# Performance work log

Measured on AMD Instinct MI355X. Metric: run time of the kernel, lower is better.

The kernel has to match this reference:

```python
import jax, jax.numpy as jnp
import numpy as np

N_NODES = 100000
N_EDGES = 3200000
NUM_TYPES = 8
TYPE_DIM = 16
IN_DIM = 5
HID = 64
HEADS = 2
OUT = 64
LN_EPS = 1e-5
NEG_SLOPE = 0.2


def segment_softmax(logits, seg, num_segments):
    # logits: [E, H], seg: [E] destination ids
    m = jax.ops.segment_max(logits, seg, num_segments=num_segments)
    m = jnp.where(jnp.isfinite(m), m, 0.0)
    e = jnp.exp(logits - m[seg])
    s = jax.ops.segment_sum(e, seg, num_segments=num_segments)
    return e / (s[seg] + 1e-16)


def gat_conv(x, W, a_src, a_dst, b, src, dst, n_nodes, heads, ch):
    # x: [N, F_in], W: [F_in, heads*ch], a_src/a_dst: [heads, ch], b: [heads*ch]
    h = (x @ W).reshape(n_nodes, heads, ch)            # [N, H, C]
    al_s = jnp.einsum('nhc,hc->nh', h, a_src)          # [N, H]
    al_d = jnp.einsum('nhc,hc->nh', h, a_dst)          # [N, H]
    e = jax.nn.leaky_relu(al_s[src] + al_d[dst], NEG_SLOPE)  # [E, H]
    alpha = segment_softmax(e, dst, n_nodes)           # [E, H]
    msg = alpha[:, :, None] * h[src]                   # [E, H, C]
    out = jax.ops.segment_sum(msg, dst, num_segments=n_nodes)  # [N, H, C]
    return out.reshape(n_nodes, heads * ch) + b


def setup_inputs() -> dict:
    key = jax.random.key(0)
    ks = jax.random.split(key, 16)
    in1 = IN_DIM + TYPE_DIM  # 21
    inp = {
        'x': jax.random.normal(ks[0], (N_NODES, IN_DIM), dtype=jnp.float32),
        'edge_index': jax.random.randint(ks[1], (2, N_EDGES), 0, N_NODES, dtype=jnp.int32),
        'type_ids': jax.random.randint(ks[2], (N_NODES,), 0, NUM_TYPES, dtype=jnp.int32),
        'type_emb': jax.random.normal(ks[3], (NUM_TYPES, TYPE_DIM), dtype=jnp.float32) * 0.3,
        'W1': jax.random.normal(ks[4], (in1, HID), dtype=jnp.float32) * (1.0 / np.sqrt(in1)),
        'a_src1': jax.random.normal(ks[5], (HEADS, HID // HEADS), dtype=jnp.float32) * 0.1,
        'a_dst1': jax.random.normal(ks[6], (HEADS, HID // HEADS), dtype=jnp.float32) * 0.1,
        'b1': jnp.zeros((HID,), dtype=jnp.float32),
        'W2': jax.random.normal(ks[7], (HID, OUT), dtype=jnp.float32) * (1.0 / np.sqrt(HID)),
        'a_src2': jax.random.normal(ks[8], (1, OUT), dtype=jnp.float32) * 0.1,
        'a_dst2': jax.random.normal(ks[9], (1, OUT), dtype=jnp.float32) * 0.1,
        'b2': jnp.zeros((OUT,), dtype=jnp.float32),
        'gamma': jnp.ones((OUT,), dtype=jnp.float32),
        'beta': jnp.zeros((OUT,), dtype=jnp.float32),
    }
    return inp


def reference(x, type_emb, W1, a_src1, a_dst1, b1, W2, a_src2, a_dst2, b2, gamma, beta, edge_index, type_ids):
    n = x.shape[0]
    # type embedding concat
    xin = jnp.concatenate([x, type_emb[type_ids]], axis=1)  # [N, 21]
    # add self loops (PyG GATConv default)
    loops = jnp.arange(n, dtype=edge_index.dtype)
    src = jnp.concatenate([edge_index[0], loops])
    dst = jnp.concatenate([edge_index[1], loops])
    h = gat_conv(xin, W1, a_src1, a_dst1, b1, src, dst, n, HEADS, HID // HEADS)
    h = jax.nn.relu(h)  # dropout = identity at inference
    h = gat_conv(h, W2, a_src2, a_dst2, b2, src, dst, n, 1, OUT)
    # LayerNorm
    mu = jnp.mean(h, axis=-1, keepdims=True)
    var = jnp.var(h, axis=-1, keepdims=True)
    return (h - mu) / jnp.sqrt(var + LN_EPS) * gamma + beta
```

## Files before the change

kernel.cpp:

```cpp
#include <hip/hip_runtime.h>
#include <hip/hip_fp16.h>

#define NEG_SLOPE 0.2f
#define BKT_SHIFT 8
#define BKT_NODES 256
#define BKT_CAP 10240
#define SRC_SHIFT 18
#define SRC_MASK 0x3FFFF
#define CHUNK 8192
#define NBMAX 512

typedef _Float16 half8 __attribute__((ext_vector_type(8)));
typedef float float4v __attribute__((ext_vector_type(4)));

__device__ __forceinline__ int wave_iscan(int v, int lane) {
#pragma unroll
    for (int off = 1; off < 64; off <<= 1) {
        int u = __shfl_up(v, off);
        if (lane >= off) v += u;
    }
    return v;
}

__global__ void k_node1(const float* __restrict__ x, const int* __restrict__ type_ids,
                        const float* __restrict__ type_emb, const float* __restrict__ W1,
                        const float* __restrict__ a_src1, const float* __restrict__ a_dst1,
                        __half2* __restrict__ h1h, float* __restrict__ als1, float* __restrict__ ald1,
                        int N)
{
    int node = blockIdx.x * 4 + (threadIdx.x >> 6);
    int j = threadIdx.x & 63;
    if (node >= N) return;

    float xin[21];
#pragma unroll
    for (int k = 0; k < 5; k++) xin[k] = x[node * 5 + k];
    int t = type_ids[node];
#pragma unroll
    for (int k = 0; k < 16; k++) xin[5 + k] = type_emb[t * 16 + k];

    float h = 0.f;
#pragma unroll
    for (int k = 0; k < 21; k++) h += xin[k] * W1[k * 64 + j];

    float hn = __shfl_xor(h, 1);
    if ((j & 1) == 0)
        h1h[node * 32 + (j >> 1)] = __floats2half2_rn(h, hn);

    int head = j >> 5, lane = j & 31;
    float ps = h * a_src1[head * 32 + lane];
    float pd = h * a_dst1[head * 32 + lane];
#pragma unroll
    for (int m = 16; m >= 1; m >>= 1) { ps += __shfl_xor(ps, m); pd += __shfl_xor(pd, m); }
    if (lane == 0) { als1[node * 2 + head] = ps; ald1[node * 2 + head] = pd; }
}

__global__ __launch_bounds__(512) void k_bucketA(
        const int* __restrict__ ei, unsigned int* __restrict__ pk,
        int* __restrict__ bcnt, int E, int NBKT)
{
    __shared__ unsigned int stage[CHUNK];
    __shared__ unsigned short stageB[CHUNK];
    __shared__ int cnt[NBMAX];
    __shared__ int excl[NBMAX];
    __shared__ int curp[NBMAX];
    __shared__ int gbase[NBMAX];
    __shared__ int wpart[8];

    int t = threadIdx.x;
    int lane = t & 63, wv = t >> 6;
    int e0 = blockIdx.x * CHUNK;
    bool vec4 = ((E & 3) == 0);

    cnt[t] = 0;
    __syncthreads();

    int4 s4[4], d4[4];
    bool val[4];

    if (vec4) {
#pragma unroll
        for (int it = 0; it < 4; it++) {
            int e = e0 + it * 2048 + t * 4;
            val[it] = (e < E);
            if (val[it]) {
                s4[it] = *(const int4*)(ei + e);
                d4[it] = *(const int4*)(ei + (size_t)E + e);
                atomicAdd(&cnt[d4[it].x >> BKT_SHIFT], 1);
                atomicAdd(&cnt[d4[it].y >> BKT_SHIFT], 1);
                atomicAdd(&cnt[d4[it].z >> BKT_SHIFT], 1);
                atomicAdd(&cnt[d4[it].w >> BKT_SHIFT], 1);
            }
        }
    } else {
        for (int i = t; i < CHUNK; i += 512) {
            int e = e0 + i;
            if (e >= E) break;
            atomicAdd(&cnt[ei[E + e] >> BKT_SHIFT], 1);
        }
    }
    __syncthreads();
    int myc = cnt[t];
    int incl = wave_iscan(myc, lane);
    if (lane == 63) wpart[wv] = incl;
    __syncthreads();
#pragma unroll
    for (int k = 0; k < 8; k++)
        if (k < wv) incl += wpart[k];
    {
        int ex = incl - myc;
        excl[t] = ex;
        curp[t] = ex;
        if (t < NBKT)
            gbase[t] = (myc > 0) ? atomicAdd(&bcnt[t], myc) : 0;
    }
    __syncthreads();
    if (vec4) {
#pragma unroll
        for (int it = 0; it < 4; it++) {
            if (!val[it]) continue;
            int ss[4] = {s4[it].x, s4[it].y, s4[it].z, s4[it].w};
            int dd[4] = {d4[it].x, d4[it].y, d4[it].z, d4[it].w};
#pragma unroll
            for (int k = 0; k < 4; k++) {
                int b = dd[k] >> BKT_SHIFT;
                int p = atomicAdd(&curp[b], 1);
                stage[p] = (unsigned)ss[k] | ((unsigned)(dd[k] & (BKT_NODES - 1)) << SRC_SHIFT);
                stageB[p] = (unsigned short)b;
            }
        }
    } else {
        for (int i = t; i < CHUNK; i += 512) {
            int e = e0 + i;
            if (e >= E) break;
            int s = ei[e], d = ei[E + e];
            int b = d >> BKT_SHIFT;
            int p = atomicAdd(&curp[b], 1);
            stage[p] = (unsigned)s | ((unsigned)(d & (BKT_NODES - 1)) << SRC_SHIFT);
            stageB[p] = (unsigned short)b;
        }
    }
    __syncthreads();
    int total = E - e0; if (total > CHUNK) total = CHUNK;
    for (int i = t; i < total; i += 512) {
        int b = stageB[i];
        int idx = gbase[b] + (i - excl[b]);
        if (idx < BKT_CAP) pk[(size_t)b * BKT_CAP + idx] = stage[i];
    }
}

__global__ __launch_bounds__(512) void k_scanb(
        const int* __restrict__ bcnt, int* __restrict__ bbase, int NBKT)
{
    __shared__ int wpart[8];
    int t = threadIdx.x;
    int lane = t & 63, wv = t >> 6;
    int v = (t < NBKT) ? min(bcnt[t], BKT_CAP) : 0;
    int incl = wave_iscan(v, lane);
    if (lane == 63) wpart[wv] = incl;
    __syncthreads();
#pragma unroll
    for (int k = 0; k < 8; k++)
        if (k < wv) incl += wpart[k];
    if (t < NBKT) bbase[t] = incl - v;
}

__global__ __launch_bounds__(512) void k_build(
        const unsigned int* __restrict__ pk, const int* __restrict__ bcnt,
        const int* __restrict__ bbase,
        int* __restrict__ rs, int* __restrict__ cur,
        int* __restrict__ ssrc, int N)
{
    __shared__ int cnt[BKT_NODES];
    __shared__ int cursor[BKT_NODES];
    __shared__ int wpart[4];
    int b = blockIdx.x;
    int t = threadIdx.x;
    int lane = t & 63, wv = t >> 6;
    int nb = min(bcnt[b], BKT_CAP);
    int bs = bbase[b];

    if (t < BKT_NODES) cnt[t] = 0;
    __syncthreads();

    const unsigned int* mypk = pk + (size_t)b * BKT_CAP;
    int nb4 = nb & ~3;
    for (int e = t * 4; e < nb4; e += 2048) {
        uint4 v = *(const uint4*)(mypk + e);
        atomicAdd(&cnt[v.x >> SRC_SHIFT], 1);
        atomicAdd(&cnt[v.y >> SRC_SHIFT], 1);
        atomicAdd(&cnt[v.z >> SRC_SHIFT], 1);
        atomicAdd(&cnt[v.w >> SRC_SHIFT], 1);
    }
    for (int e = nb4 + t; e < nb; e += 512) {
        atomicAdd(&cnt[mypk[e] >> SRC_SHIFT], 1);
    }
    __syncthreads();
    if (t < BKT_NODES) {
        int myc = cnt[t];
        int incl = wave_iscan(myc, lane);
        if (lane == 63) wpart[wv] = incl;
        __syncthreads();
#pragma unroll
        for (int k = 0; k < 4; k++)
            if (k < wv) incl += wpart[k];
        int ex = incl - myc;
        cursor[t] = ex;
        int node = (b << BKT_SHIFT) + t;
        if (node < N) { rs[node] = bs + ex; cur[node] = bs + ex + myc; }
    } else {
        __syncthreads();
    }
    __syncthreads();
    for (int e = t; e < nb; e += 512) {
        unsigned int w = mypk[e];
        int p = atomicAdd(&cursor[w >> SRC_SHIFT], 1);
        ssrc[bs + p] = (int)(w & SRC_MASK);
    }
}

__global__ void k_gather1(const int* __restrict__ rs, const int* __restrict__ cur,
                          const int* __restrict__ ssrc, const float4* __restrict__ h4,
                          const float* __restrict__ als1, const float* __restrict__ ald1,
                          const float* __restrict__ b1, float4* __restrict__ h2h4, int N)
{
    int t = threadIdx.x;
    int l = t & 63;
    int q = l & 15;
    int i = q & 7;
    int hlf = q >> 3;
    int grpbase = l & 48;
    int head = i >> 2;

    int node = blockIdx.x * 16 + (t >> 4);
    bool live = node < N;
    int node_c = live ? node : (N - 1);

    int beg = rs[node_c];
    int cnt = live ? (cur[node_c] - beg) : 0;

    float ad0 = ald1[node_c * 2 + 0];
    float ad1 = ald1[node_c * 2 + 1];
    float ad = head ? ad1 : ad0;

    int mc = cnt;
    mc = max(mc, __shfl_xor(mc, 16));
    mc = max(mc, __shfl_xor(mc, 32));

    float acc[8];
#pragma unroll
    for (int k = 0; k < 8; k++) acc[k] = 0.f;
    float wsum = 0.f;

    for (int b = 0; b < mc; b += 16) {
        int slot = b + q;
        bool valid = slot < cnt;
        int idx = valid ? (beg + slot) : 0;
        int s = ssrc[idx];
        if (!valid) s = node_c;
        float2 al = *(const float2*)(als1 + (size_t)s * 2);
        float lg0 = al.x + ad0; lg0 = (lg0 >= 0.f) ? lg0 : NEG_SLOPE * lg0;
        float lg1 = al.y + ad1; lg1 = (lg1 >= 0.f) ? lg1 : NEG_SLOPE * lg1;
        float w0 = valid ? __expf(lg0) : 0.f;
        float w1 = valid ? __expf(lg1) : 0.f;
        __half2 wp = __floats2half2_rn(w0, w1);
        unsigned wpi = *(unsigned*)&wp;

#pragma unroll
        for (int r = 0; r < 8; r++) {
            int srcl = grpbase + hlf * 8 + r;
            int sr = __shfl(s, srcl);
            unsigned wri = __shfl(wpi, srcl);
            __half2 wh = *(__half2*)&wri;
            float w = head ? __high2float(wh) : __low2float(wh);
            float4 rv = h4[(size_t)sr * 8 + i];
            const __half* hp = (const __half*)&rv;
#pragma unroll
            for (int k = 0; k < 8; k++)
                acc[k] = fmaf(w, __half2float(hp[k]), acc[k]);
            wsum += w;
        }
    }

#pragma unroll
    for (int k = 0; k < 8; k++) acc[k] += __shfl_xor(acc[k], 8);
    wsum += __shfl_xor(wsum, 8);

    {
        float lg = als1[node_c * 2 + head] + ad;
        lg = (lg >= 0.f) ? lg : NEG_SLOPE * lg;
        float w = __expf(lg);
        float4 rv = h4[(size_t)node_c * 8 + i];
        const __half* hp = (const __half*)&rv;
#pragma unroll
        for (int k = 0; k < 8; k++)
            acc[k] = fmaf(w, __half2float(hp[k]), acc[k]);
        wsum += w;
    }

    float inv = 1.f / (wsum + 1e-16f);
    if (live && hlf == 0) {
        union { float4 f4; __half2 h2[4]; } u;
#pragma unroll
        for (int c = 0; c < 4; c++) {
            float v0 = fmaxf(acc[2*c]   * inv + b1[i * 8 + 2*c],     0.f);
            float v1 = fmaxf(acc[2*c+1] * inv + b1[i * 8 + 2*c + 1], 0.f);
            u.h2[c] = __floats2half2_rn(v0, v1);
        }
        h2h4[(size_t)node * 8 + i] = u.f4;
    }
}

__global__ __launch_bounds__(256) void k_node2m(
        const _Float16* __restrict__ h2h, const float* __restrict__ W2,
        const float* __restrict__ a_src2, const float* __restrict__ a_dst2,
        _Float16* __restrict__ h3h, float* __restrict__ als2, float* __restrict__ ald2, int N)
{
    __shared__ _Float16 w2t[64][72];
    __shared__ float h3t[4][16][65];
    int t = threadIdx.x;
    for (int e = t; e < 4096; e += 256) {
        int k = e >> 6, n = e & 63;
        w2t[n][k] = (_Float16)W2[e];
    }
    __syncthreads();

    int w = t >> 6, l = t & 63;
    int l15 = l & 15, quad = l >> 4;
    int nodebase = blockIdx.x * 64 + w * 16;

    int arow = nodebase + l15;
    if (arow >= N) arow = N - 1;
    const half8* ap = (const half8*)(h2h + (size_t)arow * 64 + quad * 8);
    half8 a0 = ap[0];
    half8 a1 = ap[4];
    float4v accs[4];
#pragma unroll
    for (int nt = 0; nt < 4; nt++) {
        half8 b0 = *(const half8*)(&w2t[nt * 16 + l15][quad * 8]);
        half8 b1 = *(const half8*)(&w2t[nt * 16 + l15][32 + quad * 8]);
        float4v c = {0.f, 0.f, 0.f, 0.f};
        c = __builtin_amdgcn_mfma_f32_16x16x32_f16(a0, b0, c, 0, 0, 0);
        c = __builtin_amdgcn_mfma_f32_16x16x32_f16(a1, b1, c, 0, 0, 0);
        accs[nt] = c;
    }
#pragma unroll
    for (int nt = 0; nt < 4; nt++)
#pragma unroll
        for (int r = 0; r < 4; r++)
            h3t[w][quad * 4 + r][nt * 16 + l15] = accs[nt][r];
    __syncthreads();

    int m = l >> 2, part = l & 3;
    int g = blockIdx.x * 64 + w * 16 + m;
    float ps = 0.f, pd = 0.f;
    union { float4 f4[2]; _Float16 h[16]; } u;
#pragma unroll
    for (int c = 0; c < 16; c++) {
        float v = h3t[w][m][part * 16 + c];
        ps += v * a_src2[part * 16 + c];
        pd += v * a_dst2[part * 16 + c];
        u.h[c] = (_Float16)v;
    }
    if (g < N) {
        float4* dst = (float4*)(h3h + (size_t)g * 64) + part * 2;
        dst[0] = u.f4[0];
        dst[1] = u.f4[1];
    }
    ps += __shfl_xor(ps, 1); ps += __shfl_xor(ps, 2);
    pd += __shfl_xor(pd, 1); pd += __shfl_xor(pd, 2);
    if (part == 0 && g < N) { als2[g] = ps; ald2[g] = pd; }
}

__global__ void k_gather2(const int* __restrict__ rs, const int* __restrict__ cur,
                          const int* __restrict__ ssrc, const float4* __restrict__ h4,
                          const float* __restrict__ als2, const float* __restrict__ ald2,
                          const float* __restrict__ b2, const float* __restrict__ gamma,
                          const float* __restrict__ beta, float* __restrict__ out, int N)
{
    int t = threadIdx.x;
    int l = t & 63;
    int q = l & 15;
    int i = q & 7;
    int hlf = q >> 3;
    int grpbase = l & 48;

    int node = blockIdx.x * 16 + (t >> 4);
    bool live = node < N;
    int node_c = live ? node : (N - 1);

    int beg = rs[node_c];
    int cnt = live ? (cur[node_c] - beg) : 0;
    float ad = ald2[node_c];

    int mc = cnt;
    mc = max(mc, __shfl_xor(mc, 16));
    mc = max(mc, __shfl_xor(mc, 32));

    float acc[8];
#pragma unroll
    for (int k = 0; k < 8; k++) acc[k] = 0.f;
    float wsum = 0.f;

    for (int b = 0; b < mc; b += 16) {
        int slot = b + q;
        bool valid = slot < cnt;
        int idx = valid ? (beg + slot) : 0;
        int s = ssrc[idx];
        if (!valid) s = node_c;
        float lg = als2[s] + ad;
        lg = (lg >= 0.f) ? lg : NEG_SLOPE * lg;
        float w = valid ? __expf(lg) : 0.f;

#pragma unroll
        for (int r = 0; r < 8; r++) {
            int srcl = grpbase + hlf * 8 + r;
            int sr = __shfl(s, srcl);
            float wr = __shfl(w, srcl);
            float4 rv = h4[(size_t)sr * 8 + i];
            const __half* hp = (const __half*)&rv;
#pragma unroll
            for (int k = 0; k < 8; k++)
                acc[k] = fmaf(wr, __half2float(hp[k]), acc[k]);
            wsum += wr;
        }
    }

#pragma unroll
    for (int k = 0; k < 8; k++) acc[k] += __shfl_xor(acc[k], 8);
    wsum += __shfl_xor(wsum, 8);

    {
        float lg = als2[node_c] + ad;
        lg = (lg >= 0.f) ? lg : NEG_SLOPE * lg;
        float w = __expf(lg);
        float4 rv = h4[(size_t)node_c * 8 + i];
        const __half* hp = (const __half*)&rv;
#pragma unroll
        for (int k = 0; k < 8; k++)
            acc[k] = fmaf(w, __half2float(hp[k]), acc[k]);
        wsum += w;
    }

    float inv = 1.f / (wsum + 1e-16f);
    float o[8];
    float s = 0.f;
#pragma unroll
    for (int k = 0; k < 8; k++) { o[k] = acc[k] * inv + b2[i * 8 + k]; s += o[k]; }
    s += __shfl_xor(s, 1); s += __shfl_xor(s, 2); s += __shfl_xor(s, 4);
    float mu = s * (1.f / 64.f);
    float v = 0.f;
#pragma unroll
    for (int k = 0; k < 8; k++) { float d = o[k] - mu; v += d * d; }
    v += __shfl_xor(v, 1); v += __shfl_xor(v, 2); v += __shfl_xor(v, 4);
    v *= (1.f / 64.f);
    float rstd = rsqrtf(v + 1e-5f);
    if (live && hlf == 0) {
        float res[8];
#pragma unroll
        for (int k = 0; k < 8; k++)
            res[k] = (o[k] - mu) * rstd * gamma[i * 8 + k] + beta[i * 8 + k];
        float4* op = (float4*)(out + (size_t)node * 64 + i * 8);
        op[0] = make_float4(res[0], res[1], res[2], res[3]);
        op[1] = make_float4(res[4], res[5], res[6], res[7]);
    }
}

extern "C" void kernel_launch(void* const* d_in, const int* in_sizes, int n_in,
                              void* d_out, int out_size, void* d_ws, size_t ws_size,
                              hipStream_t stream) {
    const float* x        = (const float*)d_in[0];
    const int*   ei       = (const int*)  d_in[1];
    const int*   type_ids = (const int*)  d_in[2];
    const float* type_emb = (const float*)d_in[3];
    const float* W1       = (const float*)d_in[4];
    const float* a_src1   = (const float*)d_in[5];
    const float* a_dst1   = (const float*)d_in[6];
    const float* b1       = (const float*)d_in[7];
    const float* W2       = (const float*)d_in[8];
    const float* a_src2   = (const float*)d_in[9];
    const float* a_dst2   = (const float*)d_in[10];
    const float* b2       = (const float*)d_in[11];
    const float* gamma    = (const float*)d_in[12];
    const float* beta     = (const float*)d_in[13];

    int N = in_sizes[0] / 5;
    int E = in_sizes[1] / 2;
    int NBKT = (N + BKT_NODES - 1) >> BKT_SHIFT;

    char* base = (char*)d_ws;
    size_t off = 0;
    auto carve = [&](size_t bytes) { void* p = base + off; off += (bytes + 255) & ~(size_t)255; return p; };
    __half2* h1h = (__half2*)carve((size_t)N * 64 * sizeof(__half));
    size_t pk_bytes = (size_t)NBKT * BKT_CAP * sizeof(unsigned int);
    size_t h23_bytes = 2 * (size_t)N * 64 * sizeof(__half);
    char* uni = (char*)carve(pk_bytes > h23_bytes ? pk_bytes : h23_bytes);
    _Float16* h2h = (_Float16*)uni;
    _Float16* h3h = (_Float16*)(uni + (size_t)N * 64 * sizeof(__half));
    unsigned int* pk = (unsigned int*)uni;
    float* als1  = (float*)carve((size_t)N * 2 * sizeof(float));
    float* ald1  = (float*)carve((size_t)N * 2 * sizeof(float));
    float* als2  = (float*)carve((size_t)N * sizeof(float));
    float* ald2  = (float*)carve((size_t)N * sizeof(float));
    int*   rs    = (int*)carve((size_t)N * sizeof(int));
    int*   cur   = (int*)carve((size_t)N * sizeof(int));
    int*   bcnt  = (int*)carve(1024 * sizeof(int));
    int*   bbase = (int*)carve(1024 * sizeof(int));
    int*   ssrc  = (int*)carve((size_t)E * sizeof(int) + 256);

    dim3 tb(256);
    dim3 tb512(512);

    k_node1<<<dim3((N + 3) / 4), tb, 0, stream>>>(x, type_ids, type_emb, W1, a_src1, a_dst1,
                                                  h1h, als1, ald1, N);

    hipMemsetAsync(bcnt, 0, NBKT * sizeof(int), stream);
    k_bucketA<<<dim3((E + CHUNK - 1) / CHUNK), tb512, 0, stream>>>(ei, pk, bcnt, E, NBKT);
    k_scanb<<<dim3(1), tb512, 0, stream>>>(bcnt, bbase, NBKT);
    k_build<<<dim3(NBKT), tb512, 0, stream>>>(pk, bcnt, bbase, rs, cur, ssrc, N);

    dim3 ng((N + 15) / 16);
    k_gather1<<<ng, tb, 0, stream>>>(rs, cur, ssrc, (const float4*)h1h, als1, ald1, b1,
                                     (float4*)h2h, N);
    k_node2m<<<dim3((N + 63) / 64), tb, 0, stream>>>(h2h, W2, a_src2, a_dst2,
                                                     h3h, als2, ald2, N);
    k_gather2<<<ng, tb, 0, stream>>>(rs, cur, ssrc, (const float4*)h3h, als2, ald2, b2,
                                     gamma, beta, (float*)d_out, N);
}
```

Measured before the change: 308.9 us.

## Fuse layer-2 projection into gather1 and fold bucket scan into build

Merges the second-layer linear transform (MFMA) and attention-logit computation into the first gather kernel via shared memory, so the intermediate h2 buffer is never written to or read from global memory. Removes the separate bucket-scan kernel by having each build block reduce prefix counts itself, and zeroes bucket counters inside the first node kernel instead of using a memset. This trades fewer launches and less memory traffic for per-block W2 staging, more shared memory and barriers in the latency-bound gather, and redundant prefix reductions.

Result: faster. 301.0 us (-2.5%).

```diff
diff --git a/kernel.cpp b/kernel.cpp
--- a/kernel.cpp
+++ b/kernel.cpp
@@ -26,8 +26,11 @@
                         const float* __restrict__ type_emb, const float* __restrict__ W1,
                         const float* __restrict__ a_src1, const float* __restrict__ a_dst1,
                         __half2* __restrict__ h1h, float* __restrict__ als1, float* __restrict__ ald1,
-                        int N)
+                        int* __restrict__ bcnt, int N)
 {
+    if (blockIdx.x == 0) {
+        for (int z = threadIdx.x; z < 1024; z += 256) bcnt[z] = 0;
+    }
     int node = blockIdx.x * 4 + (threadIdx.x >> 6);
     int j = threadIdx.x & 63;
     if (node >= N) return;
@@ -149,39 +152,30 @@
     }
 }
 
-__global__ __launch_bounds__(512) void k_scanb(
-        const int* __restrict__ bcnt, int* __restrict__ bbase, int NBKT)
-{
-    __shared__ int wpart[8];
-    int t = threadIdx.x;
-    int lane = t & 63, wv = t >> 6;
-    int v = (t < NBKT) ? min(bcnt[t], BKT_CAP) : 0;
-    int incl = wave_iscan(v, lane);
-    if (lane == 63) wpart[wv] = incl;
-    __syncthreads();
-#pragma unroll
-    for (int k = 0; k < 8; k++)
-        if (k < wv) incl += wpart[k];
-    if (t < NBKT) bbase[t] = incl - v;
-}
-
 __global__ __launch_bounds__(512) void k_build(
         const unsigned int* __restrict__ pk, const int* __restrict__ bcnt,
-        const int* __restrict__ bbase,
         int* __restrict__ rs, int* __restrict__ cur,
         int* __restrict__ ssrc, int N)
 {
     __shared__ int cnt[BKT_NODES];
     __shared__ int cursor[BKT_NODES];
+    __shared__ int red[512];
     __shared__ int wpart[4];
     int b = blockIdx.x;
     int t = threadIdx.x;
     int lane = t & 63, wv = t >> 6;
     int nb = min(bcnt[b], BKT_CAP);
-    int bs = bbase[b];
-
+
+    int part = 0;
+    for (int i = t; i < b; i += 512) part += min(bcnt[i], BKT_CAP);
+    red[t] = part;
     if (t < BKT_NODES) cnt[t] = 0;
     __syncthreads();
+    for (int off = 256; off; off >>= 1) {
+        if (t < off) red[t] += red[t + off];
+        __syncthreads();
+    }
+    int bs = red[0];
 
     const unsigned int* mypk = pk + (size_t)b * BKT_CAP;
     int nb4 = nb & ~3;
@@ -219,20 +213,34 @@
     }
 }
 
-__global__ void k_gather1(const int* __restrict__ rs, const int* __restrict__ cur,
-                          const int* __restrict__ ssrc, const float4* __restrict__ h4,
-                          const float* __restrict__ als1, const float* __restrict__ ald1,
-                          const float* __restrict__ b1, float4* __restrict__ h2h4, int N)
+__global__ __launch_bounds__(256) void k_gather1m(
+        const int* __restrict__ rs, const int* __restrict__ cur,
+        const int* __restrict__ ssrc, const float4* __restrict__ h4,
+        const float* __restrict__ als1, const float* __restrict__ ald1,
+        const float* __restrict__ b1, const float* __restrict__ W2,
+        const float* __restrict__ a_src2, const float* __restrict__ a_dst2,
+        _Float16* __restrict__ h3h, float* __restrict__ als2,
+        float* __restrict__ ald2, int N)
 {
+    __shared__ _Float16 w2t[64][72];
+    __shared__ float4 h2t[128];
+    __shared__ float h3t[16][65];
+
     int t = threadIdx.x;
+    for (int e = t; e < 4096; e += 256) {
+        int kk = e >> 6, nn = e & 63;
+        w2t[nn][kk] = (_Float16)W2[e];
+    }
+
     int l = t & 63;
     int q = l & 15;
     int i = q & 7;
     int hlf = q >> 3;
     int grpbase = l & 48;
     int head = i >> 2;
-
-    int node = blockIdx.x * 16 + (t >> 4);
+    int nl = t >> 4;
+
+    int node = blockIdx.x * 16 + nl;
     bool live = node < N;
     int node_c = live ? node : (N - 1);
 
@@ -252,8 +260,8 @@
     for (int k = 0; k < 8; k++) acc[k] = 0.f;
     float wsum = 0.f;
 
-    for (int b = 0; b < mc; b += 16) {
-        int slot = b + q;
+    for (int bb = 0; bb < mc; bb += 16) {
+        int slot = bb + q;
         bool valid = slot < cnt;
         int idx = valid ? (beg + slot) : 0;
         int s = ssrc[idx];
@@ -299,76 +307,50 @@
     }
 
     float inv = 1.f / (wsum + 1e-16f);
-    if (live && hlf == 0) {
+    if (hlf == 0) {
         union { float4 f4; __half2 h2[4]; } u;
 #pragma unroll
-        for (int c = 0; c < 4; c++) {
-            float v0 = fmaxf(acc[2*c]   * inv + b1[i * 8 + 2*c],     0.f);
-            float v1 = fmaxf(acc[2*c+1] * inv + b1[i * 8 + 2*c + 1], 0.f);
-            u.h2[c] = __floats2half2_rn(v0, v1);
-        }
-        h2h4[(size_t)node * 8 + i] = u.f4;
-    }
-}
-
-__global__ __launch_bounds__(256) void k_node2m(
-        const _Float16* __restrict__ h2h, const float* __restrict__ W2,
-        const float* __restrict__ a_src2, const float* __restrict__ a_dst2,
-        _Float16* __restrict__ h3h, float* __restrict__ als2, float* __restrict__ ald2, int N)
-{
-    __shared__ _Float16 w2t[64][72];
-    __shared__ float h3t[4][16][65];
-    int t = threadIdx.x;
-    for (int e = t; e < 4096; e += 256) {
-        int k = e >> 6, n = e & 63;
-        w2t[n][k] = (_Float16)W2[e];
-    }
-    __syncthreads();
-
-    int w = t >> 6, l = t & 63;
+        for (int c4 = 0; c4 < 4; c4++) {
+            float v0 = fmaxf(acc[2*c4]   * inv + b1[i * 8 + 2*c4],     0.f);
+            float v1 = fmaxf(acc[2*c4+1] * inv + b1[i * 8 + 2*c4 + 1], 0.f);
+            u.h2[c4] = __floats2half2_rn(v0, v1);
+        }
+        h2t[nl * 8 + i] = u.f4;
+    }
+    __syncthreads();
+
+    int wv = t >> 6;
     int l15 = l & 15, quad = l >> 4;
-    int nodebase = blockIdx.x * 64 + w * 16;
-
-    int arow = nodebase + l15;
-    if (arow >= N) arow = N - 1;
-    const half8* ap = (const half8*)(h2h + (size_t)arow * 64 + quad * 8);
-    half8 a0 = ap[0];
-    half8 a1 = ap[4];
-    float4v accs[4];
-#pragma unroll
-    for (int nt = 0; nt < 4; nt++) {
-        half8 b0 = *(const half8*)(&w2t[nt * 16 + l15][quad * 8]);
-        half8 b1 = *(const half8*)(&w2t[nt * 16 + l15][32 + quad * 8]);
-        float4v c = {0.f, 0.f, 0.f, 0.f};
-        c = __builtin_amdgcn_mfma_f32_16x16x32_f16(a0, b0, c, 0, 0, 0);
-        c = __builtin_amdgcn_mfma_f32_16x16x32_f16(a1, b1, c, 0, 0, 0);
-        accs[nt] = c;
-    }
-#pragma unroll
-    for (int nt = 0; nt < 4; nt++)
-#pragma unroll
-        for (int r = 0; r < 4; r++)
-            h3t[w][quad * 4 + r][nt * 16 + l15] = accs[nt][r];
-    __syncthreads();
-
-    int m = l >> 2, part = l & 3;
-    int g = blockIdx.x * 64 + w * 16 + m;
+    const _Float16* h2p = (const _Float16*)h2t;
+    half8 a0 = *(const half8*)(h2p + l15 * 64 + quad * 8);
+    half8 a1 = *(const half8*)(h2p + l15 * 64 + 32 + quad * 8);
+    half8 bf0 = *(const half8*)(&w2t[wv * 16 + l15][quad * 8]);
+    half8 bf1 = *(const half8*)(&w2t[wv * 16 + l15][32 + quad * 8]);
+    float4v cacc = {0.f, 0.f, 0.f, 0.f};
+    cacc = __builtin_amdgcn_mfma_f32_16x16x32_f16(a0, bf0, cacc, 0, 0, 0);
+    cacc = __builtin_amdgcn_mfma_f32_16x16x32_f16(a1, bf1, cacc, 0, 0, 0);
+#pragma unroll
+    for (int r = 0; r < 4; r++)
+        h3t[quad * 4 + r][wv * 16 + l15] = cacc[r];
+    __syncthreads();
+
+    int m = t >> 4, part = t & 15;
+    int g = blockIdx.x * 16 + m;
     float ps = 0.f, pd = 0.f;
-    union { float4 f4[2]; _Float16 h[16]; } u;
-#pragma unroll
-    for (int c = 0; c < 16; c++) {
-        float v = h3t[w][m][part * 16 + c];
-        ps += v * a_src2[part * 16 + c];
-        pd += v * a_dst2[part * 16 + c];
-        u.h[c] = (_Float16)v;
-    }
-    if (g < N) {
-        float4* dst = (float4*)(h3h + (size_t)g * 64) + part * 2;
-        dst[0] = u.f4[0];
-        dst[1] = u.f4[1];
-    }
+    union { float2 f2; _Float16 h[4]; } u2;
+#pragma unroll
+    for (int cc = 0; cc < 4; cc++) {
+        float v = h3t[m][part * 4 + cc];
+        ps += v * a_src2[part * 4 + cc];
+        pd += v * a_dst2[part * 4 + cc];
+        u2.h[cc] = (_Float16)v;
+    }
+    if (g < N)
+        *(float2*)(h3h + (size_t)g * 64 + part * 4) = u2.f2;
     ps += __shfl_xor(ps, 1); ps += __shfl_xor(ps, 2);
+    ps += __shfl_xor(ps, 4); ps += __shfl_xor(ps, 8);
     pd += __shfl_xor(pd, 1); pd += __shfl_xor(pd, 2);
+    pd += __shfl_xor(pd, 4); pd += __shfl_xor(pd, 8);
     if (part == 0 && g < N) { als2[g] = ps; ald2[g] = pd; }
 }
 
@@ -493,11 +475,10 @@
     auto carve = [&](size_t bytes) { void* p = base + off; off += (bytes + 255) & ~(size_t)255; return p; };
     __half2* h1h = (__half2*)carve((size_t)N * 64 * sizeof(__half));
     size_t pk_bytes = (size_t)NBKT * BKT_CAP * sizeof(unsigned int);
-    size_t h23_bytes = 2 * (size_t)N * 64 * sizeof(__half);
-    char* uni = (char*)carve(pk_bytes > h23_bytes ? pk_bytes : h23_bytes);
-    _Float16* h2h = (_Float16*)uni;
-    _Float16* h3h = (_Float16*)(uni + (size_t)N * 64 * sizeof(__half));
+    size_t h3_bytes = (size_t)N * 64 * sizeof(__half);
+    char* uni = (char*)carve(pk_bytes > h3_bytes ? pk_bytes : h3_bytes);
     unsigned int* pk = (unsigned int*)uni;
+    _Float16* h3h = (_Float16*)uni;
     float* als1  = (float*)carve((size_t)N * 2 * sizeof(float));
     float* ald1  = (float*)carve((size_t)N * 2 * sizeof(float));
     float* als2  = (float*)carve((size_t)N * sizeof(float));
@@ -505,25 +486,20 @@
     int*   rs    = (int*)carve((size_t)N * sizeof(int));
     int*   cur   = (int*)carve((size_t)N * sizeof(int));
     int*   bcnt  = (int*)carve(1024 * sizeof(int));
-    int*   bbase = (int*)carve(1024 * sizeof(int));
     int*   ssrc  = (int*)carve((size_t)E * sizeof(int) + 256);
 
     dim3 tb(256);
     dim3 tb512(512);
 
     k_node1<<<dim3((N + 3) / 4), tb, 0, stream>>>(x, type_ids, type_emb, W1, a_src1, a_dst1,
-                                                  h1h, als1, ald1, N);
-
-    hipMemsetAsync(bcnt, 0, NBKT * sizeof(int), stream);
+                                                  h1h, als1, ald1, bcnt, N);
+
     k_bucketA<<<dim3((E + CHUNK - 1) / CHUNK), tb512, 0, stream>>>(ei, pk, bcnt, E, NBKT);
-    k_scanb<<<dim3(1), tb512, 0, stream>>>(bcnt, bbase, NBKT);
-    k_build<<<dim3(NBKT), tb512, 0, stream>>>(pk, bcnt, bbase, rs, cur, ssrc, N);
+    k_build<<<dim3(NBKT), tb512, 0, stream>>>(pk, bcnt, rs, cur, ssrc, N);
 
     dim3 ng((N + 15) / 16);
-    k_gather1<<<ng, tb, 0, stream>>>(rs, cur, ssrc, (const float4*)h1h, als1, ald1, b1,
-                                     (float4*)h2h, N);
-    k_node2m<<<dim3((N + 63) / 64), tb, 0, stream>>>(h2h, W2, a_src2, a_dst2,
-                                                     h3h, als2, ald2, N);
+    k_gather1m<<<ng, tb, 0, stream>>>(rs, cur, ssrc, (const float4*)h1h, als1, ald1, b1,
+                                      W2, a_src2, a_dst2, h3h, als2, ald2, N);
     k_gather2<<<ng, tb, 0, stream>>>(rs, cur, ssrc, (const float4*)h3h, als2, ald2, b2,
                                      gamma, beta, (float*)d_out, N);
 }
```

## Fuse CSR build with layer-1 gather and drop scan kernel and memset

Applied to the files above, without the earlier changes.

Merges the per-bucket CSR build kernel with the first GAT gather, so each 512-thread block builds its bucket's adjacency and then aggregates its 256 destination nodes. Each block now sums the preceding bucket counts itself, which replaces the separate scan kernel. The counter memset moves into block 0 of the node kernel. This removes two launches and the memset, and reuses the shared-memory counts and offsets; in exchange the gather runs on only about 391 blocks instead of about 6250, which risks poor latency hiding. h2h also gets its own buffer instead of aliasing pk.

New measurement: 310.1 us. No clear change (+0.4%).

```diff
diff --git a/kernel.cpp b/kernel.cpp
--- a/kernel.cpp
+++ b/kernel.cpp
@@ -26,8 +26,11 @@
                         const float* __restrict__ type_emb, const float* __restrict__ W1,
                         const float* __restrict__ a_src1, const float* __restrict__ a_dst1,
                         __half2* __restrict__ h1h, float* __restrict__ als1, float* __restrict__ ald1,
-                        int N)
+                        int* __restrict__ bcnt, int N)
 {
+    if (blockIdx.x == 0) {
+        for (int z = threadIdx.x; z < 1024; z += 256) bcnt[z] = 0;
+    }
     int node = blockIdx.x * 4 + (threadIdx.x >> 6);
     int j = threadIdx.x & 63;
     if (node >= N) return;
@@ -149,39 +152,36 @@
     }
 }
 
-__global__ __launch_bounds__(512) void k_scanb(
-        const int* __restrict__ bcnt, int* __restrict__ bbase, int NBKT)
-{
-    __shared__ int wpart[8];
-    int t = threadIdx.x;
-    int lane = t & 63, wv = t >> 6;
-    int v = (t < NBKT) ? min(bcnt[t], BKT_CAP) : 0;
-    int incl = wave_iscan(v, lane);
-    if (lane == 63) wpart[wv] = incl;
-    __syncthreads();
-#pragma unroll
-    for (int k = 0; k < 8; k++)
-        if (k < wv) incl += wpart[k];
-    if (t < NBKT) bbase[t] = incl - v;
-}
-
-__global__ __launch_bounds__(512) void k_build(
+__global__ __launch_bounds__(512) void k_gbs1(
         const unsigned int* __restrict__ pk, const int* __restrict__ bcnt,
-        const int* __restrict__ bbase,
-        int* __restrict__ rs, int* __restrict__ cur,
-        int* __restrict__ ssrc, int N)
+        const float4* __restrict__ h4, const float* __restrict__ als1,
+        const float* __restrict__ ald1, const float* __restrict__ b1,
+        int* __restrict__ rs, int* __restrict__ cur, int* __restrict__ ssrc,
+        float4* __restrict__ h2h4, int N)
 {
     __shared__ int cnt[BKT_NODES];
     __shared__ int cursor[BKT_NODES];
+    __shared__ int nodebeg[BKT_NODES];
+    __shared__ int red[512];
     __shared__ int wpart[4];
+
     int b = blockIdx.x;
     int t = threadIdx.x;
     int lane = t & 63, wv = t >> 6;
     int nb = min(bcnt[b], BKT_CAP);
-    int bs = bbase[b];
-
+    int nbase = b << BKT_SHIFT;
+    int nn = min(BKT_NODES, N - nbase);
+
+    int part = 0;
+    for (int i2 = t; i2 < b; i2 += 512) part += min(bcnt[i2], BKT_CAP);
+    red[t] = part;
     if (t < BKT_NODES) cnt[t] = 0;
     __syncthreads();
+    for (int off = 256; off; off >>= 1) {
+        if (t < off) red[t] += red[t + off];
+        __syncthreads();
+    }
+    int bs = red[0];
 
     const unsigned int* mypk = pk + (size_t)b * BKT_CAP;
     int nb4 = nb & ~3;
@@ -206,7 +206,8 @@
             if (k < wv) incl += wpart[k];
         int ex = incl - myc;
         cursor[t] = ex;
-        int node = (b << BKT_SHIFT) + t;
+        nodebeg[t] = bs + ex;
+        int node = nbase + t;
         if (node < N) { rs[node] = bs + ex; cur[node] = bs + ex + myc; }
     } else {
         __syncthreads();
@@ -217,97 +218,91 @@
         int p = atomicAdd(&cursor[w >> SRC_SHIFT], 1);
         ssrc[bs + p] = (int)(w & SRC_MASK);
     }
-}
-
-__global__ void k_gather1(const int* __restrict__ rs, const int* __restrict__ cur,
-                          const int* __restrict__ ssrc, const float4* __restrict__ h4,
-                          const float* __restrict__ als1, const float* __restrict__ ald1,
-                          const float* __restrict__ b1, float4* __restrict__ h2h4, int N)
-{
-    int t = threadIdx.x;
+    __syncthreads();
+
     int l = t & 63;
-    int q = l & 15;
-    int i = q & 7;
-    int hlf = q >> 3;
+    int q = l & 15, i = q & 7, hlf = q >> 3;
     int grpbase = l & 48;
     int head = i >> 2;
-
-    int node = blockIdx.x * 16 + (t >> 4);
-    bool live = node < N;
-    int node_c = live ? node : (N - 1);
-
-    int beg = rs[node_c];
-    int cnt = live ? (cur[node_c] - beg) : 0;
-
-    float ad0 = ald1[node_c * 2 + 0];
-    float ad1 = ald1[node_c * 2 + 1];
-    float ad = head ? ad1 : ad0;
-
-    int mc = cnt;
-    mc = max(mc, __shfl_xor(mc, 16));
-    mc = max(mc, __shfl_xor(mc, 32));
-
-    float acc[8];
-#pragma unroll
-    for (int k = 0; k < 8; k++) acc[k] = 0.f;
-    float wsum = 0.f;
-
-    for (int b = 0; b < mc; b += 16) {
-        int slot = b + q;
-        bool valid = slot < cnt;
-        int idx = valid ? (beg + slot) : 0;
-        int s = ssrc[idx];
-        if (!valid) s = node_c;
-        float2 al = *(const float2*)(als1 + (size_t)s * 2);
-        float lg0 = al.x + ad0; lg0 = (lg0 >= 0.f) ? lg0 : NEG_SLOPE * lg0;
-        float lg1 = al.y + ad1; lg1 = (lg1 >= 0.f) ? lg1 : NEG_SLOPE * lg1;
-        float w0 = valid ? __expf(lg0) : 0.f;
-        float w1 = valid ? __expf(lg1) : 0.f;
-        __half2 wp = __floats2half2_rn(w0, w1);
-        unsigned wpi = *(unsigned*)&wp;
-
-#pragma unroll
-        for (int r = 0; r < 8; r++) {
-            int srcl = grpbase + hlf * 8 + r;
-            int sr = __shfl(s, srcl);
-            unsigned wri = __shfl(wpi, srcl);
-            __half2 wh = *(__half2*)&wri;
-            float w = head ? __high2float(wh) : __low2float(wh);
-            float4 rv = h4[(size_t)sr * 8 + i];
+    int g = t >> 4;
+
+    for (int ln = g; ln < BKT_NODES; ln += 32) {
+        bool live = ln < nn;
+        int lnc = live ? ln : (nn - 1);
+        int node = nbase + lnc;
+        int beg = nodebeg[lnc];
+        int cnt_n = live ? cnt[lnc] : 0;
+
+        float ad0 = ald1[node * 2 + 0];
+        float ad1 = ald1[node * 2 + 1];
+        float ad = head ? ad1 : ad0;
+
+        int mc = cnt_n;
+        mc = max(mc, __shfl_xor(mc, 16));
+        mc = max(mc, __shfl_xor(mc, 32));
+
+        float acc[8];
+#pragma unroll
+        for (int k = 0; k < 8; k++) acc[k] = 0.f;
+        float wsum = 0.f;
+
+        for (int bb = 0; bb < mc; bb += 16) {
+            int slot = bb + q;
+            bool valid = slot < cnt_n;
+            int idx = valid ? (beg + slot) : 0;
+            int s = ssrc[idx];
+            if (!valid) s = node;
+            float2 al = *(const float2*)(als1 + (size_t)s * 2);
+            float lg0 = al.x + ad0; lg0 = (lg0 >= 0.f) ? lg0 : NEG_SLOPE * lg0;
+            float lg1 = al.y + ad1; lg1 = (lg1 >= 0.f) ? lg1 : NEG_SLOPE * lg1;
+            float w0 = valid ? __expf(lg0) : 0.f;
+            float w1 = valid ? __expf(lg1) : 0.f;
+            __half2 wp = __floats2half2_rn(w0, w1);
+            unsigned wpi = *(unsigned*)&wp;
+
+#pragma unroll
+            for (int r = 0; r < 8; r++) {
+                int srcl = grpbase + hlf * 8 + r;
+                int sr = __shfl(s, srcl);
+                unsigned wri = __shfl(wpi, srcl);
+                __half2 wh = *(__half2*)&wri;
+                float w = head ? __high2float(wh) : __low2float(wh);
+                float4 rv = h4[(size_t)sr * 8 + i];
+                const __half* hp = (const __half*)&rv;
+#pragma unroll
+                for (int k = 0; k < 8; k++)
+                    acc[k] = fmaf(w, __half2float(hp[k]), acc[k]);
+                wsum += w;
+            }
+        }
+
+#pragma unroll
+        for (int k = 0; k < 8; k++) acc[k] += __shfl_xor(acc[k], 8);
+        wsum += __shfl_xor(wsum, 8);
+
+        {
+            float lg = als1[node * 2 + head] + ad;
+            lg = (lg >= 0.f) ? lg : NEG_SLOPE * lg;
+            float w = __expf(lg);
+            float4 rv = h4[(size_t)node * 8 + i];
             const __half* hp = (const __half*)&rv;
 #pragma unroll
             for (int k = 0; k < 8; k++)
                 acc[k] = fmaf(w, __half2float(hp[k]), acc[k]);
             wsum += w;
         }
-    }
-
-#pragma unroll
-    for (int k = 0; k < 8; k++) acc[k] += __shfl_xor(acc[k], 8);
-    wsum += __shfl_xor(wsum, 8);
-
-    {
-        float lg = als1[node_c * 2 + head] + ad;
-        lg = (lg >= 0.f) ? lg : NEG_SLOPE * lg;
-        float w = __expf(lg);
-        float4 rv = h4[(size_t)node_c * 8 + i];
-        const __half* hp = (const __half*)&rv;
-#pragma unroll
-        for (int k = 0; k < 8; k++)
-            acc[k] = fmaf(w, __half2float(hp[k]), acc[k]);
-        wsum += w;
-    }
-
-    float inv = 1.f / (wsum + 1e-16f);
-    if (live && hlf == 0) {
-        union { float4 f4; __half2 h2[4]; } u;
-#pragma unroll
-        for (int c = 0; c < 4; c++) {
-            float v0 = fmaxf(acc[2*c]   * inv + b1[i * 8 + 2*c],     0.f);
-            float v1 = fmaxf(acc[2*c+1] * inv + b1[i * 8 + 2*c + 1], 0.f);
-            u.h2[c] = __floats2half2_rn(v0, v1);
-        }
-        h2h4[(size_t)node * 8 + i] = u.f4;
+
+        float inv = 1.f / (wsum + 1e-16f);
+        if (live && hlf == 0) {
+            union { float4 f4; __half2 h2[4]; } u;
+#pragma unroll
+            for (int c4 = 0; c4 < 4; c4++) {
+                float v0 = fmaxf(acc[2*c4]   * inv + b1[i * 8 + 2*c4],     0.f);
+                float v1 = fmaxf(acc[2*c4+1] * inv + b1[i * 8 + 2*c4 + 1], 0.f);
+                u.h2[c4] = __floats2half2_rn(v0, v1);
+            }
+            h2h4[(size_t)node * 8 + i] = u.f4;
+        }
     }
 }
 
@@ -493,11 +488,11 @@
     auto carve = [&](size_t bytes) { void* p = base + off; off += (bytes + 255) & ~(size_t)255; return p; };
     __half2* h1h = (__half2*)carve((size_t)N * 64 * sizeof(__half));
     size_t pk_bytes = (size_t)NBKT * BKT_CAP * sizeof(unsigned int);
-    size_t h23_bytes = 2 * (size_t)N * 64 * sizeof(__half);
-    char* uni = (char*)carve(pk_bytes > h23_bytes ? pk_bytes : h23_bytes);
-    _Float16* h2h = (_Float16*)uni;
-    _Float16* h3h = (_Float16*)(uni + (size_t)N * 64 * sizeof(__half));
+    size_t h3_bytes = (size_t)N * 64 * sizeof(__half);
+    char* uni = (char*)carve(pk_bytes > h3_bytes ? pk_bytes : h3_bytes);
     unsigned int* pk = (unsigned int*)uni;
+    _Float16* h3h = (_Float16*)uni;
+    _Float16* h2h = (_Float16*)carve((size_t)N * 64 * sizeof(__half));
     float* als1  = (float*)carve((size_t)N * 2 * sizeof(float));
     float* ald1  = (float*)carve((size_t)N * 2 * sizeof(float));
     float* als2  = (float*)carve((size_t)N * sizeof(float));
@@ -505,25 +500,23 @@
     int*   rs    = (int*)carve((size_t)N * sizeof(int));
     int*   cur   = (int*)carve((size_t)N * sizeof(int));
     int*   bcnt  = (int*)carve(1024 * sizeof(int));
-    int*   bbase = (int*)carve(1024 * sizeof(int));
     int*   ssrc  = (int*)carve((size_t)E * sizeof(int) + 256);
 
     dim3 tb(256);
     dim3 tb512(512);
 
     k_node1<<<dim3((N + 3) / 4), tb, 0, stream>>>(x, type_ids, type_emb, W1, a_src1, a_dst1,
-                                                  h1h, als1, ald1, N);
-
-    hipMemsetAsync(bcnt, 0, NBKT * sizeof(int), stream);
+                                                  h1h, als1, ald1, bcnt, N);
+
     k_bucketA<<<dim3((E + CHUNK - 1) / CHUNK), tb512, 0, stream>>>(ei, pk, bcnt, E, NBKT);
-    k_scanb<<<dim3(1), tb512, 0, stream>>>(bcnt, bbase, NBKT);
-    k_build<<<dim3(NBKT), tb512, 0, stream>>>(pk, bcnt, bbase, rs, cur, ssrc, N);
-
-    dim3 ng((N + 15) / 16);
-    k_gather1<<<ng, tb, 0, stream>>>(rs, cur, ssrc, (const float4*)h1h, als1, ald1, b1,
-                                     (float4*)h2h, N);
+
+    k_gbs1<<<dim3(NBKT), tb512, 0, stream>>>(pk, bcnt, (const float4*)h1h, als1, ald1, b1,
+                                             rs, cur, ssrc, (float4*)h2h, N);
+
     k_node2m<<<dim3((N + 63) / 64), tb, 0, stream>>>(h2h, W2, a_src2, a_dst2,
                                                      h3h, als2, ald2, N);
+
+    dim3 ng((N + 15) / 16);
     k_gather2<<<ng, tb, 0, stream>>>(rs, cur, ssrc, (const float4*)h3h, als2, ald2, b2,
                                      gamma, beta, (float*)d_out, N);
 }
```
